# Kernel optimization log

Hardware: AMD Instinct MI355X
Metric: run time of the kernel (lower is better)

Reference implementation:

```python
import jax, jax.numpy as jnp
import numpy as np

N_NODES = 50000
N_EDGES = 1600000
N_FEATURES = 1433
HIDDEN = 256
N_CLASSES = 7


def setup_inputs() -> dict:
    key = jax.random.key(0)
    ks = jax.random.split(key, 5)
    x = jax.random.normal(ks[0], (N_NODES, N_FEATURES), dtype=jnp.float32)
    edge_index = jax.random.randint(ks[1], (2, N_EDGES), 0, N_NODES, dtype=jnp.int64)
    # Glorot-style init like PyG's Linear inside GCNConv
    W1 = jax.random.normal(ks[2], (N_FEATURES, HIDDEN), dtype=jnp.float32) * (1.0 / np.sqrt(N_FEATURES))
    b1 = jnp.zeros((HIDDEN,), dtype=jnp.float32)
    W2 = jax.random.normal(ks[3], (HIDDEN, N_CLASSES), dtype=jnp.float32) * (1.0 / np.sqrt(HIDDEN))
    b2 = jnp.zeros((N_CLASSES,), dtype=jnp.float32)
    return {"x": x, "edge_index": edge_index, "W1": W1, "b1": b1, "W2": W2, "b2": b2}


def _gcn_conv(x, W, b, src, dst, n_nodes):
    """PyG GCNConv: add self-loops, symmetric deg^{-1/2} norm, linear, scatter-add, +bias."""
    h = x @ W  # [N, out]
    loop = jnp.arange(n_nodes, dtype=src.dtype)
    src2 = jnp.concatenate([src, loop])
    dst2 = jnp.concatenate([dst, loop])
    ones = jnp.ones(src2.shape[0], dtype=h.dtype)
    deg = jax.ops.segment_sum(ones, dst2, num_segments=n_nodes)
    dinv = jnp.where(deg > 0, jax.lax.rsqrt(deg), 0.0)
    norm = dinv[src2] * dinv[dst2]  # [E+N]
    msg = h[src2] * norm[:, None]   # gather + scale
    out = jax.ops.segment_sum(msg, dst2, num_segments=n_nodes)
    return out + b


def reference(x, edge_index, W1, b1, W2, b2):
    src, dst = edge_index[0], edge_index[1]
    h = _gcn_conv(x, W1, b1, src, dst, N_NODES)
    h = jax.nn.relu(h)
    # dropout p=0.5 is identity in eval mode (training=False)
    out = _gcn_conv(h, W2, b2, src, dst, N_NODES)
    return out
```

## Files before the change

kernel.cpp:

```cpp
#include <hip/hip_runtime.h>
#include <hip/hip_bf16.h>


#define N_NODES_   50000
#define NB_ROWS_   50048
#define N_EDGES_   1600000
#define N_FEAT_    1433
#define K_PAD_     1440
#define HIDDEN_    256
#define N_CLASSES_ 7
#define NPART_     ((N_NODES_ + 255) / 256)
#define NT_        (K_PAD_ / 32)

typedef __attribute__((ext_vector_type(8))) short short8;
typedef __attribute__((ext_vector_type(8))) unsigned short ushort8;
typedef __attribute__((ext_vector_type(4))) float f32x4;
typedef unsigned int u32;
typedef unsigned short u16;

__device__ __forceinline__ u16 f2bf(float f) {
    __hip_bfloat16 h = __float2bfloat16(f);
    return *(u16*)&h;
}
__device__ __forceinline__ float bf2f(u16 u) {
    return __uint_as_float((u32)u << 16);
}

__global__ void deg_kernel(const int* __restrict__ dst, int* __restrict__ deg) {
    int i = blockIdx.x * blockDim.x + threadIdx.x;
    if (i < N_EDGES_) atomicAdd(&deg[dst[i]], 1);
}

__global__ void dinv_kernel(const int* __restrict__ deg, float* __restrict__ dinv) {
    int i = blockIdx.x * blockDim.x + threadIdx.x;
    if (i < N_NODES_) dinv[i] = rsqrtf((float)(deg[i] + 1));
}

__global__ __launch_bounds__(256) void scan1_kernel(const int* __restrict__ deg,
                                                    int* __restrict__ partial) {
    __shared__ int ws[4];
    int t = threadIdx.x, b = blockIdx.x;
    int idx = b * 256 + t;
    int v = (idx < N_NODES_) ? deg[idx] : 0;
    #pragma unroll
    for (int off = 32; off > 0; off >>= 1) v += __shfl_down(v, off, 64);
    if ((t & 63) == 0) ws[t >> 6] = v;
    __syncthreads();
    if (t == 0) partial[b] = ws[0] + ws[1] + ws[2] + ws[3];
}

__global__ __launch_bounds__(256) void scan2_kernel(int* __restrict__ partial,
                                                    int* __restrict__ blk_off) {
    __shared__ int sh[256];
    int t = threadIdx.x;
    int v = (t < NPART_) ? partial[t] : 0;
    sh[t] = v;
    __syncthreads();
    #pragma unroll
    for (int off = 1; off < 256; off <<= 1) {
        int a = (t >= off) ? sh[t - off] : 0;
        __syncthreads();
        sh[t] += a;
        __syncthreads();
    }
    if (t < NPART_) blk_off[t] = sh[t] - v;
}

__global__ __launch_bounds__(256) void scan3_kernel(const int* __restrict__ deg,
                                                    const int* __restrict__ blk_off,
                                                    int* __restrict__ row_ptr,
                                                    int* __restrict__ cursor) {
    __shared__ int sh[256];
    int t = threadIdx.x, b = blockIdx.x;
    int idx = b * 256 + t;
    int v = (idx < N_NODES_) ? deg[idx] : 0;
    sh[t] = v;
    __syncthreads();
    #pragma unroll
    for (int off = 1; off < 256; off <<= 1) {
        int a = (t >= off) ? sh[t - off] : 0;
        __syncthreads();
        sh[t] += a;
        __syncthreads();
    }
    if (idx < N_NODES_) {
        int rp = blk_off[b] + sh[t] - v;
        row_ptr[idx] = rp;
        cursor[idx]  = rp;
    }
    if (idx == 0) row_ptr[N_NODES_] = N_EDGES_;
}

__global__ void csr_scatter_kernel(const int* __restrict__ src, const int* __restrict__ dst,
                                   int* __restrict__ cursor, int* __restrict__ csr_src) {
    int i = blockIdx.x * blockDim.x + threadIdx.x;
    if (i >= N_EDGES_) return;
    int d = dst[i];
    int pos = atomicAdd(&cursor[d], 1);
    csr_src[pos] = src[i];
}

__global__ void w1t_kernel(const float* __restrict__ W1, u16* __restrict__ W1T) {
    int gid = blockIdx.x * blockDim.x + threadIdx.x;
    if (gid >= HIDDEN_ * K_PAD_) return;
    int k = gid % K_PAD_, n = gid / K_PAD_;
    float v = (k < N_FEAT_) ? W1[(long)k * HIDDEN_ + n] : 0.f;
    W1T[(long)n * K_PAD_ + k] = f2bf(v);
}

__global__ __launch_bounds__(256) void gemm1_fused(const float* __restrict__ X,
                                                   const u16* __restrict__ BT,
                                                   const float* __restrict__ dinv,
                                                   u16* __restrict__ C) {
    const int tid  = threadIdx.x;
    const int lane = tid & 63;
    const int wv   = tid >> 6;
    const int row0 = blockIdx.x * 32;

    const int fm = lane & 15;
    const int q  = lane >> 4;

    f32x4 acc[2][4] = {};

    const int r0 = min(row0 + fm,      N_NODES_ - 1);
    const int r1 = min(row0 + 16 + fm, N_NODES_ - 1);
    const float* xb0 = X + (long)r0 * N_FEAT_ + q * 8;
    const float* xb1 = X + (long)r1 * N_FEAT_ + q * 8;
    const u16*   bb  = BT + (long)(wv * 64 + fm) * K_PAD_ + q * 8;

    float  na0[8], na1[8];
    short8 nb[4];
    short8 af[2], bfr[4];

    #pragma unroll
    for (int j = 0; j < 8; j++) { na0[j] = xb0[j]; na1[j] = xb1[j]; }
    #pragma unroll
    for (int ni = 0; ni < 4; ni++)
        nb[ni] = *(const short8*)(bb + (long)ni * 16 * K_PAD_);
    #pragma unroll
    for (int j = 0; j < 8; j++) { af[0][j] = (short)f2bf(na0[j]); af[1][j] = (short)f2bf(na1[j]); }
    #pragma unroll
    for (int ni = 0; ni < 4; ni++) bfr[ni] = nb[ni];

    for (int t = 0; t < NT_ - 1; ++t) {
        const int k0n = (t + 1) * 32;
        if (t < NT_ - 2) {
            #pragma unroll
            for (int j = 0; j < 8; j++) { na0[j] = xb0[k0n + j]; na1[j] = xb1[k0n + j]; }
        } else {
            #pragma unroll
            for (int j = 0; j < 8; j++) {
                bool ok = (k0n + q * 8 + j) < N_FEAT_;
                na0[j] = ok ? xb0[k0n + j] : 0.f;
                na1[j] = ok ? xb1[k0n + j] : 0.f;
            }
        }
        #pragma unroll
        for (int ni = 0; ni < 4; ni++)
            nb[ni] = *(const short8*)(bb + (long)ni * 16 * K_PAD_ + k0n);
        #pragma unroll
        for (int mi = 0; mi < 2; mi++)
            #pragma unroll
            for (int ni = 0; ni < 4; ni++)
                acc[mi][ni] = __builtin_amdgcn_mfma_f32_16x16x32_bf16(af[mi], bfr[ni], acc[mi][ni], 0, 0, 0);
        #pragma unroll
        for (int j = 0; j < 8; j++) { af[0][j] = (short)f2bf(na0[j]); af[1][j] = (short)f2bf(na1[j]); }
        #pragma unroll
        for (int ni = 0; ni < 4; ni++) bfr[ni] = nb[ni];
    }
    #pragma unroll
    for (int mi = 0; mi < 2; mi++)
        #pragma unroll
        for (int ni = 0; ni < 4; ni++)
            acc[mi][ni] = __builtin_amdgcn_mfma_f32_16x16x32_bf16(af[mi], bfr[ni], acc[mi][ni], 0, 0, 0);

    const int q4 = q * 4;
    #pragma unroll
    for (int mi = 0; mi < 2; mi++) {
        #pragma unroll
        for (int r = 0; r < 4; r++) {
            int gm = row0 + mi * 16 + q4 + r;
            if (gm < N_NODES_) {
                float sc = dinv[gm];
                #pragma unroll
                for (int ni = 0; ni < 4; ni++) {
                    int gn = wv * 64 + ni * 16 + fm;
                    C[(long)gm * HIDDEN_ + gn] = f2bf(acc[mi][ni][r] * sc);
                }
            }
        }
    }
}

__global__ __launch_bounds__(256) void agg_gemm2_kernel(const u16* __restrict__ h1s,
                                                        const int* __restrict__ row_ptr,
                                                        const int* __restrict__ csr_src,
                                                        const float* __restrict__ dinv,
                                                        const float* __restrict__ b1,
                                                        const float* __restrict__ W2,
                                                        float* __restrict__ h2s) {
    __shared__ float w2s[HIDDEN_ * N_CLASSES_];
    __shared__ float b1s[HIDDEN_];
    int tid = threadIdx.x;
    for (int i = tid; i < HIDDEN_ * N_CLASSES_; i += 256) w2s[i] = W2[i];
    for (int i = tid; i < HIDDEN_; i += 256) b1s[i] = b1[i];
    __syncthreads();

    int wave = tid >> 6;
    int lane = tid & 63;
    int node = blockIdx.x * 4 + wave;
    if (node >= N_NODES_) return;

    int e0 = row_ptr[node], e1 = row_ptr[node + 1];
    float ax = 0.f, ay = 0.f, az = 0.f, aw = 0.f;

    int sL = (e0 + lane < e1) ? csr_src[e0 + lane] : N_NODES_;
    for (int base = e0; base < e1; base += 64) {
        int sCur = sL;
        int nb = base + 64;
        if (nb < e1) sL = (nb + lane < e1) ? csr_src[nb + lane] : N_NODES_;
        int cnt8 = (min(64, e1 - base) + 7) & ~7;
        for (int j = 0; j < cnt8; j += 8) {
            #pragma unroll
            for (int t = 0; t < 8; t++) {
                int s = __shfl(sCur, j + t, 64);
                ushort4 u = ((const ushort4*)(h1s + (long)s * HIDDEN_))[lane];
                ax += bf2f(u.x);
                ay += bf2f(u.y);
                az += bf2f(u.z);
                aw += bf2f(u.w);
            }
        }
    }
    float nd = dinv[node];
    ushort4 su = ((const ushort4*)(h1s + (long)node * HIDDEN_))[lane];
    float xv[4];
    xv[0] = fmaxf((ax + bf2f(su.x)) * nd + b1s[lane * 4 + 0], 0.f);
    xv[1] = fmaxf((ay + bf2f(su.y)) * nd + b1s[lane * 4 + 1], 0.f);
    xv[2] = fmaxf((az + bf2f(su.z)) * nd + b1s[lane * 4 + 2], 0.f);
    xv[3] = fmaxf((aw + bf2f(su.w)) * nd + b1s[lane * 4 + 3], 0.f);

    float p[N_CLASSES_];
    #pragma unroll
    for (int c = 0; c < N_CLASSES_; c++) {
        float a = 0.f;
        #pragma unroll
        for (int i = 0; i < 4; i++)
            a += xv[i] * w2s[(lane * 4 + i) * N_CLASSES_ + c];
        p[c] = a;
    }
    #pragma unroll
    for (int off = 32; off > 0; off >>= 1)
        #pragma unroll
        for (int c = 0; c < N_CLASSES_; c++)
            p[c] += __shfl_down(p[c], off, 64);
    if (lane == 0) {
        #pragma unroll
        for (int c = 0; c < N_CLASSES_; c++)
            h2s[(long)node * 8 + c] = p[c] * nd;
    }
}

__global__ void out_kernel(const float* __restrict__ h2s,
                           const int* __restrict__ row_ptr,
                           const int* __restrict__ csr_src,
                           const float* __restrict__ dinv,
                           const float* __restrict__ b2,
                           float* __restrict__ out) {
    long gid = (long)blockIdx.x * blockDim.x + threadIdx.x;
    int node = (int)(gid >> 3);
    int c = (int)(gid & 7);
    if (node >= N_NODES_ || c >= N_CLASSES_) return;
    int e0 = row_ptr[node], e1 = row_ptr[node + 1];
    float acc = 0.f;
    for (int e = e0; e < e1; e += 4) {
        int s0 = csr_src[e];
        int s1 = (e + 1 < e1) ? csr_src[e + 1] : N_NODES_;
        int s2 = (e + 2 < e1) ? csr_src[e + 2] : N_NODES_;
        int s3 = (e + 3 < e1) ? csr_src[e + 3] : N_NODES_;
        float v0 = h2s[(long)s0 * 8 + c];
        float v1 = h2s[(long)s1 * 8 + c];
        float v2 = h2s[(long)s2 * 8 + c];
        float v3 = h2s[(long)s3 * 8 + c];
        acc += (v0 + v1) + (v2 + v3);
    }
    float nd = dinv[node];
    out[(long)node * N_CLASSES_ + c] =
        (acc + h2s[(long)node * 8 + c]) * nd + b2[c];
}

extern "C" void kernel_launch(void* const* d_in, const int* in_sizes, int n_in,
                              void* d_out, int out_size, void* d_ws, size_t ws_size,
                              hipStream_t stream) {
    const float* x   = (const float*)d_in[0];
    const int*   ei  = (const int*)d_in[1];
    const int*   src = ei;
    const int*   dst = ei + N_EDGES_;
    const float* W1  = (const float*)d_in[2];
    const float* b1  = (const float*)d_in[3];
    const float* W2  = (const float*)d_in[4];
    const float* b2  = (const float*)d_in[5];
    float* out = (float*)d_out;

    char* ws = (char*)d_ws;
    size_t off = 0;
    auto alloc = [&](size_t bytes) { void* p = ws + off; off = (off + bytes + 255) & ~(size_t)255; return p; };
    u16*   h1s     = (u16*)alloc((size_t)(N_NODES_ + 1) * HIDDEN_ * 2);
    u16*   w1t     = (u16*)alloc((size_t)HIDDEN_ * K_PAD_ * 2);
    float* h2s     = (float*)alloc((size_t)(N_NODES_ + 1) * 8 * 4);
    int*   deg     = (int*)alloc((size_t)N_NODES_ * 4);
    float* dinv    = (float*)alloc((size_t)N_NODES_ * 4);
    int*   row_ptr = (int*)alloc((size_t)(N_NODES_ + 1) * 4);
    int*   cursor  = (int*)alloc((size_t)N_NODES_ * 4);
    int*   csr_src = (int*)alloc((size_t)N_EDGES_ * 4);
    int*   partial = (int*)alloc((size_t)NPART_ * 4);
    int*   blk_off = (int*)alloc((size_t)NPART_ * 4);

    hipMemsetAsync(deg, 0, (size_t)N_NODES_ * 4, stream);
    hipMemsetAsync(h1s + (size_t)N_NODES_ * HIDDEN_, 0, HIDDEN_ * 2, stream);
    hipMemsetAsync(h2s + (size_t)N_NODES_ * 8, 0, 8 * 4, stream);

    deg_kernel<<<(N_EDGES_ + 255) / 256, 256, 0, stream>>>(dst, deg);
    dinv_kernel<<<(N_NODES_ + 255) / 256, 256, 0, stream>>>(deg, dinv);
    scan1_kernel<<<NPART_, 256, 0, stream>>>(deg, partial);
    scan2_kernel<<<1, 256, 0, stream>>>(partial, blk_off);
    scan3_kernel<<<NPART_, 256, 0, stream>>>(deg, blk_off, row_ptr, cursor);
    csr_scatter_kernel<<<(N_EDGES_ + 255) / 256, 256, 0, stream>>>(src, dst, cursor, csr_src);

    w1t_kernel<<<(HIDDEN_ * K_PAD_ + 255) / 256, 256, 0, stream>>>(W1, w1t);

    gemm1_fused<<<NB_ROWS_ / 32, 256, 0, stream>>>(x, w1t, dinv, h1s);

    agg_gemm2_kernel<<<(N_NODES_ + 3) / 4, 256, 0, stream>>>(h1s, row_ptr, csr_src, dinv, b1, W2, h2s);

    long out_threads = (long)N_NODES_ * 8;
    out_kernel<<<(unsigned)((out_threads + 255) / 256), 256, 0, stream>>>(h2s, row_ptr, csr_src, dinv, b2, out);
}
```

Baseline: 905.0 us.

## Stage X rows in LDS as bf16 and triple-buffer B loads in gemm1

```diff
diff --git a/kernel.cpp b/kernel.cpp
--- a/kernel.cpp
+++ b/kernel.cpp
@@ -11,6 +11,8 @@
 #define N_CLASSES_ 7
 #define NPART_     ((N_NODES_ + 255) / 256)
 #define NT_        (K_PAD_ / 32)
+#define BM1_       16
+#define APAD_      1448
 
 typedef __attribute__((ext_vector_type(8))) short short8;
 typedef __attribute__((ext_vector_type(8))) unsigned short ushort8;
@@ -108,85 +110,91 @@
     W1T[(long)n * K_PAD_ + k] = f2bf(v);
 }
 
-__global__ __launch_bounds__(256) void gemm1_fused(const float* __restrict__ X,
-                                                   const u16* __restrict__ BT,
-                                                   const float* __restrict__ dinv,
-                                                   u16* __restrict__ C) {
+__device__ __forceinline__ void loadB4(const u16* bb, int koff, short8* dst) {
+    #pragma unroll
+    for (int ni = 0; ni < 4; ni++)
+        dst[ni] = *(const short8*)(bb + (long)ni * 16 * K_PAD_ + koff);
+}
+__device__ __forceinline__ void mfma4(const short8& a, const short8* b, f32x4* acc) {
+    #pragma unroll
+    for (int ni = 0; ni < 4; ni++)
+        acc[ni] = __builtin_amdgcn_mfma_f32_16x16x32_bf16(a, b[ni], acc[ni], 0, 0, 0);
+}
+
+__global__ __launch_bounds__(256, 3) void gemm1_fused(const float* __restrict__ X,
+                                                      const u16* __restrict__ BT,
+                                                      const float* __restrict__ dinv,
+                                                      u16* __restrict__ C) {
+    __shared__ u16 As[BM1_ * APAD_];
+
     const int tid  = threadIdx.x;
     const int lane = tid & 63;
     const int wv   = tid >> 6;
-    const int row0 = blockIdx.x * 32;
+    const int row0 = blockIdx.x * BM1_;
+
+    for (int rr = 0; rr < BM1_; ++rr) {
+        const float* xr = X + (long)min(row0 + rr, N_NODES_ - 1) * N_FEAT_;
+        u16* lr = &As[rr * APAD_];
+        #pragma unroll
+        for (int it = 0; it < 6; ++it) {
+            int k = it * 256 + tid;
+            if (k < K_PAD_) {
+                float v = (k < N_FEAT_) ? xr[k] : 0.f;
+                lr[k] = f2bf(v);
+            }
+        }
+    }
+    __syncthreads();
 
     const int fm = lane & 15;
     const int q  = lane >> 4;
 
-    f32x4 acc[2][4] = {};
-
-    const int r0 = min(row0 + fm,      N_NODES_ - 1);
-    const int r1 = min(row0 + 16 + fm, N_NODES_ - 1);
-    const float* xb0 = X + (long)r0 * N_FEAT_ + q * 8;
-    const float* xb1 = X + (long)r1 * N_FEAT_ + q * 8;
-    const u16*   bb  = BT + (long)(wv * 64 + fm) * K_PAD_ + q * 8;
-
-    float  na0[8], na1[8];
-    short8 nb[4];
-    short8 af[2], bfr[4];
-
-    #pragma unroll
-    for (int j = 0; j < 8; j++) { na0[j] = xb0[j]; na1[j] = xb1[j]; }
-    #pragma unroll
-    for (int ni = 0; ni < 4; ni++)
-        nb[ni] = *(const short8*)(bb + (long)ni * 16 * K_PAD_);
-    #pragma unroll
-    for (int j = 0; j < 8; j++) { af[0][j] = (short)f2bf(na0[j]); af[1][j] = (short)f2bf(na1[j]); }
-    #pragma unroll
-    for (int ni = 0; ni < 4; ni++) bfr[ni] = nb[ni];
-
-    for (int t = 0; t < NT_ - 1; ++t) {
-        const int k0n = (t + 1) * 32;
-        if (t < NT_ - 2) {
+    f32x4 acc[4] = {};
+    const u16* bb   = BT + (long)(wv * 64 + fm) * K_PAD_ + q * 8;
+    const u16* arow = &As[fm * APAD_ + q * 8];
+
+    short8 b0[4], b1[4], b2[4];
+    loadB4(bb, 0,  b0);
+    loadB4(bb, 32, b1);
+
+    int t = 0;
+    #pragma unroll 1
+    for (int tt = 0; tt < 14; ++tt) {
+        short8 a;
+        loadB4(bb, (t + 2) * 32, b2);
+        a = *(const short8*)(arow + t * 32);
+        mfma4(a, b0, acc);
+        ++t;
+        loadB4(bb, (t + 2) * 32, b0);
+        a = *(const short8*)(arow + t * 32);
+        mfma4(a, b1, acc);
+        ++t;
+        loadB4(bb, (t + 2) * 32, b1);
+        a = *(const short8*)(arow + t * 32);
+        mfma4(a, b2, acc);
+        ++t;
+    }
+    {
+        short8 a;
+        loadB4(bb, 44 * 32, b2);
+        a = *(const short8*)(arow + 42 * 32);
+        mfma4(a, b0, acc);
+        a = *(const short8*)(arow + 43 * 32);
+        mfma4(a, b1, acc);
+        a = *(const short8*)(arow + 44 * 32);
+        mfma4(a, b2, acc);
+    }
+
+    const int q4 = q * 4;
+    #pragma unroll
+    for (int r = 0; r < 4; r++) {
+        int gm = row0 + q4 + r;
+        if (gm < N_NODES_) {
+            float sc = dinv[gm];
             #pragma unroll
-            for (int j = 0; j < 8; j++) { na0[j] = xb0[k0n + j]; na1[j] = xb1[k0n + j]; }
-        } else {
-            #pragma unroll
-            for (int j = 0; j < 8; j++) {
-                bool ok = (k0n + q * 8 + j) < N_FEAT_;
-                na0[j] = ok ? xb0[k0n + j] : 0.f;
-                na1[j] = ok ? xb1[k0n + j] : 0.f;
-            }
-        }
-        #pragma unroll
-        for (int ni = 0; ni < 4; ni++)
-            nb[ni] = *(const short8*)(bb + (long)ni * 16 * K_PAD_ + k0n);
-        #pragma unroll
-        for (int mi = 0; mi < 2; mi++)
-            #pragma unroll
-            for (int ni = 0; ni < 4; ni++)
-                acc[mi][ni] = __builtin_amdgcn_mfma_f32_16x16x32_bf16(af[mi], bfr[ni], acc[mi][ni], 0, 0, 0);
-        #pragma unroll
-        for (int j = 0; j < 8; j++) { af[0][j] = (short)f2bf(na0[j]); af[1][j] = (short)f2bf(na1[j]); }
-        #pragma unroll
-        for (int ni = 0; ni < 4; ni++) bfr[ni] = nb[ni];
-    }
-    #pragma unroll
-    for (int mi = 0; mi < 2; mi++)
-        #pragma unroll
-        for (int ni = 0; ni < 4; ni++)
-            acc[mi][ni] = __builtin_amdgcn_mfma_f32_16x16x32_bf16(af[mi], bfr[ni], acc[mi][ni], 0, 0, 0);
-
-    const int q4 = q * 4;
-    #pragma unroll
-    for (int mi = 0; mi < 2; mi++) {
-        #pragma unroll
-        for (int r = 0; r < 4; r++) {
-            int gm = row0 + mi * 16 + q4 + r;
-            if (gm < N_NODES_) {
-                float sc = dinv[gm];
-                #pragma unroll
-                for (int ni = 0; ni < 4; ni++) {
-                    int gn = wv * 64 + ni * 16 + fm;
-                    C[(long)gm * HIDDEN_ + gn] = f2bf(acc[mi][ni][r] * sc);
-                }
+            for (int ni = 0; ni < 4; ni++) {
+                int gn = wv * 64 + ni * 16 + fm;
+                C[(long)gm * HIDDEN_ + gn] = f2bf(acc[ni][r] * sc);
             }
         }
     }
@@ -329,7 +337,7 @@
 
     w1t_kernel<<<(HIDDEN_ * K_PAD_ + 255) / 256, 256, 0, stream>>>(W1, w1t);
 
-    gemm1_fused<<<NB_ROWS_ / 32, 256, 0, stream>>>(x, w1t, dinv, h1s);
+    gemm1_fused<<<NB_ROWS_ / BM1_, 256, 0, stream>>>(x, w1t, dinv, h1s);
 
     agg_gemm2_kernel<<<(N_NODES_ + 3) / 4, 256, 0, stream>>>(h1s, row_ptr, csr_src, dinv, b1, W2, h2s);
 
```

Result: slower. 987.0 us (+9.1%).
